# Optimization experiments

Hardware: AMD Instinct MI355X
Metric: run time of the kernel (lower is better)

The kernel has to match this reference:

```python
import jax, jax.numpy as jnp
import numpy as np

N_NODES = 50000


def gcn_conv(x, edge_index, W, b):
    """PyG GCNConv: add self-loops, sym-normalize, out = A_hat @ (x W) + b."""
    src, dst = edge_index[0], edge_index[1]
    n = x.shape[0]
    h = x @ W  # [N, out]
    # degree with self-loops (all edge weights = 1)
    deg = jax.ops.segment_sum(jnp.ones_like(dst, dtype=x.dtype), dst, num_segments=n) + 1.0
    dinv = jax.lax.rsqrt(deg)  # deg >= 1 so safe
    norm = dinv[src] * dinv[dst]  # [E]
    msgs = h[src] * norm[:, None]  # gather + scale
    agg = jax.ops.segment_sum(msgs, dst, num_segments=n)  # scatter-add
    agg = agg + h * (dinv * dinv)[:, None]  # self-loop term: norm_ii = dinv_i^2
    return agg + b


def setup_inputs() -> dict:
    key = jax.random.key(0)
    k_x, k_e, k_w1, k_w2 = jax.random.split(key, 4)
    in_ch, hid, out_ch = 256, 128, 128
    x = jax.random.normal(k_x, (N_NODES, in_ch), dtype=jnp.float32)
    edge_index = jax.random.randint(k_e, (2, 1_600_000), 0, N_NODES, dtype=jnp.int32)
    # Glorot-style init like PyG GCNConv
    W1 = jax.random.normal(k_w1, (in_ch, hid), dtype=jnp.float32) * (1.0 / np.sqrt(in_ch))
    b1 = jnp.zeros((hid,), dtype=jnp.float32)
    W2 = jax.random.normal(k_w2, (hid, out_ch), dtype=jnp.float32) * (1.0 / np.sqrt(hid))
    b2 = jnp.zeros((out_ch,), dtype=jnp.float32)
    return {"x": x, "edge_index": edge_index, "W1": W1, "b1": b1, "W2": W2, "b2": b2}


def reference(x, edge_index, W1, b1, W2, b2):
    # layer 1: GCNConv -> ReLU (dropout is identity in eval mode)
    h = jax.nn.relu(gcn_conv(x, edge_index, W1, b1))
    # layer 2: GCNConv -> ReLU
    out = jax.nn.relu(gcn_conv(h, edge_index, W2, b2))
    return out
```

## Files before the change

### kernel.cpp

```cpp
#include <hip/hip_runtime.h>
#include <cstdint>
#include <cstddef>


#define ELL_STRIDE 64
#define BCAP 8192
#define OVF_CAP 1024
#define PART_T 2048

typedef __attribute__((ext_vector_type(8))) short bf16x8;
typedef __attribute__((ext_vector_type(4))) float floatx4;

__device__ __forceinline__ unsigned short f2bf(float f) {
  unsigned int u = __float_as_uint(f);
  unsigned int r = (u + 0x7fffu + ((u >> 16) & 1u)) >> 16;
  return (unsigned short)r;
}
__device__ __forceinline__ float2 bfpair(unsigned int p) {
  float2 r;
  r.x = __uint_as_float(p << 16);
  r.y = __uint_as_float(p & 0xffff0000u);
  return r;
}

__global__ __launch_bounds__(256) void k_cvt_w(const float* __restrict__ W1,
                                               const float* __restrict__ W2,
                                               unsigned short* __restrict__ WT1,
                                               unsigned short* __restrict__ WT2,
                                               int* __restrict__ cursor,
                                               int* __restrict__ ovf_cnt,
                                               int NB) {
  int i = blockIdx.x * 256 + threadIdx.x;
  if (i < NB) cursor[i] = 0;
  if (i == NB) *ovf_cnt = 0;
  if (i < 128 * 256) {
    int n = i >> 8, k = i & 255;
    WT1[i] = f2bf(W1[k * 128 + n]);
  } else if (i < 128 * 256 + 128 * 128) {
    int j = i - 128 * 256;
    int n = j >> 7, k = j & 127;
    WT2[j] = f2bf(W2[k * 128 + n]);
  }
}

__global__ __launch_bounds__(256) void k_part(const int* __restrict__ src,
                                              const int* __restrict__ dst,
                                              int* __restrict__ cursor,
                                              unsigned int* __restrict__ part,
                                              int* __restrict__ ovf_cnt,
                                              int* __restrict__ ovf,
                                              int E, int NB) {
  __shared__ unsigned int stage1[PART_T];
  __shared__ unsigned int stage2[PART_T];
  __shared__ int hist[512];
  __shared__ int base_g[512];
  __shared__ int base_l[512];
  __shared__ int cl[512];
  __shared__ int sc[256];
  const int tid = threadIdx.x;
  const int e0 = blockIdx.x * PART_T;
  int valid = E - e0; if (valid > PART_T) valid = PART_T;

  hist[tid] = 0; hist[tid + 256] = 0;
  cl[tid] = 0; cl[tid + 256] = 0;
  __syncthreads();
  for (int i = tid; i < valid; i += 256) {
    int e = e0 + i;
    unsigned int v = (unsigned int)(src[e] & 0xffff) | ((unsigned int)dst[e] << 16);
    stage1[i] = v;
    atomicAdd(&hist[(v >> 16) >> 7], 1);
  }
  __syncthreads();
  for (int b = tid; b < NB; b += 256) base_g[b] = atomicAdd(&cursor[b], hist[b]);
  int h0 = hist[2 * tid], h1 = hist[2 * tid + 1];
  int pv = h0 + h1;
  sc[tid] = pv;
  __syncthreads();
  #pragma unroll
  for (int off = 1; off < 256; off <<= 1) {
    int t = (tid >= off) ? sc[tid - off] : 0;
    __syncthreads();
    sc[tid] += t;
    __syncthreads();
  }
  int excl = sc[tid] - pv;
  base_l[2 * tid] = excl;
  base_l[2 * tid + 1] = excl + h0;
  __syncthreads();
  for (int i = tid; i < valid; i += 256) {
    unsigned int v = stage1[i];
    int b = (v >> 16) >> 7;
    int pos = base_l[b] + atomicAdd(&cl[b], 1);
    stage2[pos] = v;
  }
  __syncthreads();
  for (int i = tid; i < valid; i += 256) {
    unsigned int v = stage2[i];
    int b = (v >> 16) >> 7;
    int g = base_g[b] + (i - base_l[b]);
    if (g < BCAP) {
      part[(size_t)b * BCAP + g] = v;
    } else {
      int p = atomicAdd(ovf_cnt, 1);
      if (p < OVF_CAP) { ovf[2 * p] = (int)(v & 0xffffu); ovf[2 * p + 1] = (int)(v >> 16); }
    }
  }
}

__global__ __launch_bounds__(256) void k_fill2(const unsigned int* __restrict__ part,
                                               const int* __restrict__ cursor,
                                               unsigned short* __restrict__ col,
                                               int* __restrict__ cnt,
                                               float* __restrict__ dinv,
                                               int* __restrict__ ovf_cnt,
                                               int* __restrict__ ovf, int N) {
  __shared__ unsigned short slab[128 * ELL_STRIDE];
  __shared__ int cl[128];
  const int tid = threadIdx.x;
  const int b = blockIdx.x;
  if (tid < 128) cl[tid] = 0;
  __syncthreads();
  int count = cursor[b]; if (count > BCAP) count = BCAP;
  const unsigned int* p = part + (size_t)b * BCAP;
  for (int i = tid; i < count; i += 256) {
    unsigned int v = p[i];
    int row = (v >> 16) & 127;
    int k = atomicAdd(&cl[row], 1);
    if (k < ELL_STRIDE) {
      slab[row * ELL_STRIDE + k] = (unsigned short)(v & 0xffffu);
    } else {
      int q = atomicAdd(ovf_cnt, 1);
      if (q < OVF_CAP) { ovf[2 * q] = (int)(v & 0xffffu); ovf[2 * q + 1] = (int)(v >> 16); }
    }
  }
  __syncthreads();
  uint4* d4 = (uint4*)(col + (size_t)b * 128 * ELL_STRIDE);
  const uint4* s4 = (const uint4*)slab;
  #pragma unroll
  for (int i = 0; i < (128 * ELL_STRIDE * 2) / (16 * 256); ++i)
    d4[i * 256 + tid] = s4[i * 256 + tid];
  if (tid < 128) {
    int node = b * 128 + tid;
    if (node < N) {
      int c = cl[tid];
      cnt[node] = c;
      dinv[node] = rsqrtf((float)c + 1.0f);
    }
  }
}

template <int K, bool AF32>
__global__ __launch_bounds__(256) void k_gemm_mfma(const void* __restrict__ Xv,
                                                   const unsigned short* __restrict__ WT,
                                                   const float* __restrict__ dinv,
                                                   unsigned short* __restrict__ hb,
                                                   int M) {
  constexpr int KP = K + 8;
  __shared__ unsigned short Bs[64 * KP];
  const int tid = threadIdx.x;
  const int wave = tid >> 6, lane = tid & 63;
  const int q = lane >> 4, m = lane & 15;
  const int row0 = blockIdx.x * 64 + wave * 16;
  const bool active = row0 < M;
  const int arow = row0 + m;

  floatx4 acc[8];
  #pragma unroll
  for (int nt = 0; nt < 8; ++nt) acc[nt] = (floatx4){0.f, 0.f, 0.f, 0.f};
  bf16x8 af[K / 32];

  #pragma unroll
  for (int half = 0; half < 2; ++half) {
    __syncthreads();
    for (int c = tid; c < 64 * (K / 8); c += 256) {
      int r = c / (K / 8), ko = (c % (K / 8)) * 8;
      *(uint4*)(Bs + r * KP + ko) =
          *(const uint4*)(WT + (size_t)(half * 64 + r) * K + ko);
    }
    __syncthreads();
    if (active) {
      #pragma unroll
      for (int ks = 0; ks < K / 32; ++ks) {
        const int k0 = ks * 32 + q * 8;
        if (half == 0) {
          if (AF32) {
            const float* X = (const float*)Xv;
            float4 a0 = *(const float4*)(X + (size_t)arow * K + k0);
            float4 a1 = *(const float4*)(X + (size_t)arow * K + k0 + 4);
            af[ks] = (bf16x8){(short)f2bf(a0.x), (short)f2bf(a0.y),
                              (short)f2bf(a0.z), (short)f2bf(a0.w),
                              (short)f2bf(a1.x), (short)f2bf(a1.y),
                              (short)f2bf(a1.z), (short)f2bf(a1.w)};
          } else {
            af[ks] = *(const bf16x8*)((const unsigned short*)Xv +
                                      (size_t)arow * K + k0);
          }
        }
        #pragma unroll
        for (int ntl = 0; ntl < 4; ++ntl) {
          bf16x8 bf = *(const bf16x8*)(Bs + (ntl * 16 + m) * KP + k0);
          acc[half * 4 + ntl] =
              __builtin_amdgcn_mfma_f32_16x16x32_bf16(af[ks], bf, acc[half * 4 + ntl],
                                                      0, 0, 0);
        }
      }
    }
  }
  if (!active) return;
  #pragma unroll
  for (int r = 0; r < 4; ++r) {
    int grow = row0 + q * 4 + r;
    float di = dinv[grow];
    #pragma unroll
    for (int nt = 0; nt < 8; ++nt)
      hb[(size_t)grow * 128 + nt * 16 + m] = f2bf(acc[nt][r] * di);
  }
}

template <bool BF16OUT>
__global__ __launch_bounds__(256) void k_agg(const unsigned int* __restrict__ hb,
                                             const int* __restrict__ cnt,
                                             const unsigned short* __restrict__ col,
                                             const float* __restrict__ dinv,
                                             const int* __restrict__ ovf_cnt,
                                             const int* __restrict__ ovf,
                                             const float* __restrict__ bias,
                                             void* __restrict__ outv, int n) {
  const int wave = threadIdx.x >> 6;
  const int lane = threadIdx.x & 63;
  const int d = blockIdx.x * 4 + wave;
  if (d >= n) return;

  float2 acc = bfpair(hb[(size_t)d * 64 + lane]);

  int m = cnt[d]; if (m > ELL_STRIDE) m = ELL_STRIDE;
  const unsigned short* crow = col + (size_t)d * ELL_STRIDE;
  int k = 0;
  for (; k + 16 <= m; k += 16) {
    ushort4 c0 = *(const ushort4*)(crow + k);
    ushort4 c1 = *(const ushort4*)(crow + k + 4);
    ushort4 c2 = *(const ushort4*)(crow + k + 8);
    ushort4 c3 = *(const ushort4*)(crow + k + 12);
    unsigned int p0 = hb[(size_t)c0.x * 64 + lane];
    unsigned int p1 = hb[(size_t)c0.y * 64 + lane];
    unsigned int p2 = hb[(size_t)c0.z * 64 + lane];
    unsigned int p3 = hb[(size_t)c0.w * 64 + lane];
    unsigned int p4 = hb[(size_t)c1.x * 64 + lane];
    unsigned int p5 = hb[(size_t)c1.y * 64 + lane];
    unsigned int p6 = hb[(size_t)c1.z * 64 + lane];
    unsigned int p7 = hb[(size_t)c1.w * 64 + lane];
    unsigned int p8 = hb[(size_t)c2.x * 64 + lane];
    unsigned int p9 = hb[(size_t)c2.y * 64 + lane];
    unsigned int pa = hb[(size_t)c2.z * 64 + lane];
    unsigned int pb = hb[(size_t)c2.w * 64 + lane];
    unsigned int pc = hb[(size_t)c3.x * 64 + lane];
    unsigned int pd = hb[(size_t)c3.y * 64 + lane];
    unsigned int pe = hb[(size_t)c3.z * 64 + lane];
    unsigned int pf = hb[(size_t)c3.w * 64 + lane];
    float2 v0 = bfpair(p0), v1 = bfpair(p1), v2 = bfpair(p2), v3 = bfpair(p3);
    float2 v4 = bfpair(p4), v5 = bfpair(p5), v6 = bfpair(p6), v7 = bfpair(p7);
    acc.x += v0.x + v1.x + v2.x + v3.x + v4.x + v5.x + v6.x + v7.x;
    acc.y += v0.y + v1.y + v2.y + v3.y + v4.y + v5.y + v6.y + v7.y;
    float2 v8 = bfpair(p8), v9 = bfpair(p9), va = bfpair(pa), vb = bfpair(pb);
    float2 vc = bfpair(pc), vd = bfpair(pd), ve = bfpair(pe), vf = bfpair(pf);
    acc.x += v8.x + v9.x + va.x + vb.x + vc.x + vd.x + ve.x + vf.x;
    acc.y += v8.y + v9.y + va.y + vb.y + vc.y + vd.y + ve.y + vf.y;
  }
  for (; k + 8 <= m; k += 8) {
    ushort4 ca = *(const ushort4*)(crow + k);
    ushort4 cb = *(const ushort4*)(crow + k + 4);
    unsigned int p0 = hb[(size_t)ca.x * 64 + lane];
    unsigned int p1 = hb[(size_t)ca.y * 64 + lane];
    unsigned int p2 = hb[(size_t)ca.z * 64 + lane];
    unsigned int p3 = hb[(size_t)ca.w * 64 + lane];
    unsigned int p4 = hb[(size_t)cb.x * 64 + lane];
    unsigned int p5 = hb[(size_t)cb.y * 64 + lane];
    unsigned int p6 = hb[(size_t)cb.z * 64 + lane];
    unsigned int p7 = hb[(size_t)cb.w * 64 + lane];
    float2 v0 = bfpair(p0), v1 = bfpair(p1), v2 = bfpair(p2), v3 = bfpair(p3);
    float2 v4 = bfpair(p4), v5 = bfpair(p5), v6 = bfpair(p6), v7 = bfpair(p7);
    acc.x += v0.x + v1.x + v2.x + v3.x + v4.x + v5.x + v6.x + v7.x;
    acc.y += v0.y + v1.y + v2.y + v3.y + v4.y + v5.y + v6.y + v7.y;
  }
  for (; k < m; ++k) {
    int c = crow[k];
    float2 v = bfpair(hb[(size_t)c * 64 + lane]);
    acc.x += v.x; acc.y += v.y;
  }
  int V = *ovf_cnt; if (V > OVF_CAP) V = OVF_CAP;
  for (int j = 0; j < V; ++j) {
    if (ovf[2 * j + 1] == d) {
      float2 v = bfpair(hb[(size_t)ovf[2 * j] * 64 + lane]);
      acc.x += v.x; acc.y += v.y;
    }
  }
  float di = dinv[d];
  float2 bv = *(const float2*)(bias + lane * 2);
  float rx = di * acc.x + bv.x;
  float ry = di * acc.y + bv.y;
  rx = rx > 0.f ? rx : 0.f;
  ry = ry > 0.f ? ry : 0.f;
  if (BF16OUT) {
    unsigned int pk = (unsigned int)f2bf(rx) | ((unsigned int)f2bf(ry) << 16);
    ((unsigned int*)outv)[(size_t)d * 64 + lane] = pk;
  } else {
    *(float2*)((float*)outv + (size_t)d * 128 + lane * 2) = make_float2(rx, ry);
  }
}

extern "C" void kernel_launch(void* const* d_in, const int* in_sizes, int n_in,
                              void* d_out, int out_size, void* d_ws, size_t ws_size,
                              hipStream_t stream) {
  const float* x  = (const float*)d_in[0];
  const int*   ei = (const int*)d_in[1];
  const float* W1 = (const float*)d_in[2];
  const float* b1 = (const float*)d_in[3];
  const float* W2 = (const float*)d_in[4];
  const float* b2 = (const float*)d_in[5];
  float* out = (float*)d_out;

  const int IN_CH = 256;
  const int N = in_sizes[0] / IN_CH;
  const int E = in_sizes[1] / 2;
  const int NB = (N + 127) >> 7;

  const int* src = ei;
  const int* dst = ei + E;

  char* ws = (char*)d_ws;
  size_t off = 0;
  auto carve = [&](size_t bytes) {
    void* p = ws + off;
    off += (bytes + 255) & ~(size_t)255;
    return p;
  };
  int*            cursor  = (int*)carve((size_t)NB * 4);
  int*            ovf_cnt = (int*)carve(4);
  int*            ovf     = (int*)carve((size_t)OVF_CAP * 2 * 4);
  int*            cnt     = (int*)carve((size_t)N * 4);
  float*          dinv    = (float*)carve((size_t)N * 4);
  unsigned short* col     = (unsigned short*)carve((size_t)N * ELL_STRIDE * 2);
  unsigned short* hb      = (unsigned short*)carve((size_t)N * 128 * 2);
  unsigned short* WT1     = (unsigned short*)carve(128 * 256 * 2);
  unsigned short* WT2     = (unsigned short*)carve(128 * 128 * 2);
  char*           unionp  = (char*)carve((size_t)NB * BCAP * 4);
  unsigned int*   part    = (unsigned int*)unionp;
  unsigned short* aggbuf  = (unsigned short*)unionp;

  k_cvt_w<<<(128 * 256 + 128 * 128 + 255) / 256, 256, 0, stream>>>(
      W1, W2, WT1, WT2, cursor, ovf_cnt, NB);
  k_part <<<(E + PART_T - 1) / PART_T, 256, 0, stream>>>(src, dst, cursor, part,
                                                         ovf_cnt, ovf, E, NB);
  k_fill2<<<NB, 256, 0, stream>>>(part, cursor, col, cnt, dinv, ovf_cnt, ovf, N);

  int gblocks = (N + 63) / 64;
  int ablocks = (N + 3) / 4;
  k_gemm_mfma<256, true ><<<gblocks, 256, 0, stream>>>(x, WT1, dinv, hb, N);
  k_agg<true ><<<ablocks, 256, 0, stream>>>((const unsigned int*)hb, cnt, col, dinv,
                                            ovf_cnt, ovf, b1, aggbuf, N);
  k_gemm_mfma<128, false><<<gblocks, 256, 0, stream>>>(aggbuf, WT2, dinv, hb, N);
  k_agg<false><<<ablocks, 256, 0, stream>>>((const unsigned int*)hb, cnt, col, dinv,
                                            ovf_cnt, ovf, b2, out, N);
}
```

Baseline: 262.5 us.

## Store hidden features in column-chunk slabs and split aggregation per chunk

```diff
diff --git a/kernel.cpp b/kernel.cpp
--- a/kernel.cpp
+++ b/kernel.cpp
@@ -213,7 +213,7 @@
     float di = dinv[grow];
     #pragma unroll
     for (int nt = 0; nt < 8; ++nt)
-      hb[(size_t)grow * 128 + nt * 16 + m] = f2bf(acc[nt][r] * di);
+      hb[(size_t)nt * M * 16 + (size_t)grow * 16 + m] = f2bf(acc[nt][r] * di);
   }
 }
 
@@ -226,85 +226,55 @@
                                              const int* __restrict__ ovf,
                                              const float* __restrict__ bias,
                                              void* __restrict__ outv, int n) {
-  const int wave = threadIdx.x >> 6;
-  const int lane = threadIdx.x & 63;
-  const int d = blockIdx.x * 4 + wave;
+  const int wave = threadIdx.x >> 6, lane = threadIdx.x & 63;
+  const int chunk = blockIdx.x & 7;
+  const int d = (blockIdx.x >> 3) * 4 + wave;
   if (d >= n) return;
-
-  float2 acc = bfpair(hb[(size_t)d * 64 + lane]);
+  const int e = lane >> 3, u = lane & 7;
+  const unsigned int* slab = hb + (size_t)chunk * n * 8;
 
   int m = cnt[d]; if (m > ELL_STRIDE) m = ELL_STRIDE;
-  const unsigned short* crow = col + (size_t)d * ELL_STRIDE;
-  int k = 0;
-  for (; k + 16 <= m; k += 16) {
-    ushort4 c0 = *(const ushort4*)(crow + k);
-    ushort4 c1 = *(const ushort4*)(crow + k + 4);
-    ushort4 c2 = *(const ushort4*)(crow + k + 8);
-    ushort4 c3 = *(const ushort4*)(crow + k + 12);
-    unsigned int p0 = hb[(size_t)c0.x * 64 + lane];
-    unsigned int p1 = hb[(size_t)c0.y * 64 + lane];
-    unsigned int p2 = hb[(size_t)c0.z * 64 + lane];
-    unsigned int p3 = hb[(size_t)c0.w * 64 + lane];
-    unsigned int p4 = hb[(size_t)c1.x * 64 + lane];
-    unsigned int p5 = hb[(size_t)c1.y * 64 + lane];
-    unsigned int p6 = hb[(size_t)c1.z * 64 + lane];
-    unsigned int p7 = hb[(size_t)c1.w * 64 + lane];
-    unsigned int p8 = hb[(size_t)c2.x * 64 + lane];
-    unsigned int p9 = hb[(size_t)c2.y * 64 + lane];
-    unsigned int pa = hb[(size_t)c2.z * 64 + lane];
-    unsigned int pb = hb[(size_t)c2.w * 64 + lane];
-    unsigned int pc = hb[(size_t)c3.x * 64 + lane];
-    unsigned int pd = hb[(size_t)c3.y * 64 + lane];
-    unsigned int pe = hb[(size_t)c3.z * 64 + lane];
-    unsigned int pf = hb[(size_t)c3.w * 64 + lane];
-    float2 v0 = bfpair(p0), v1 = bfpair(p1), v2 = bfpair(p2), v3 = bfpair(p3);
-    float2 v4 = bfpair(p4), v5 = bfpair(p5), v6 = bfpair(p6), v7 = bfpair(p7);
-    acc.x += v0.x + v1.x + v2.x + v3.x + v4.x + v5.x + v6.x + v7.x;
-    acc.y += v0.y + v1.y + v2.y + v3.y + v4.y + v5.y + v6.y + v7.y;
-    float2 v8 = bfpair(p8), v9 = bfpair(p9), va = bfpair(pa), vb = bfpair(pb);
-    float2 vc = bfpair(pc), vd = bfpair(pd), ve = bfpair(pe), vf = bfpair(pf);
-    acc.x += v8.x + v9.x + va.x + vb.x + vc.x + vd.x + ve.x + vf.x;
-    acc.y += v8.y + v9.y + va.y + vb.y + vc.y + vd.y + ve.y + vf.y;
-  }
-  for (; k + 8 <= m; k += 8) {
-    ushort4 ca = *(const ushort4*)(crow + k);
-    ushort4 cb = *(const ushort4*)(crow + k + 4);
-    unsigned int p0 = hb[(size_t)ca.x * 64 + lane];
-    unsigned int p1 = hb[(size_t)ca.y * 64 + lane];
-    unsigned int p2 = hb[(size_t)ca.z * 64 + lane];
-    unsigned int p3 = hb[(size_t)ca.w * 64 + lane];
-    unsigned int p4 = hb[(size_t)cb.x * 64 + lane];
-    unsigned int p5 = hb[(size_t)cb.y * 64 + lane];
-    unsigned int p6 = hb[(size_t)cb.z * 64 + lane];
-    unsigned int p7 = hb[(size_t)cb.w * 64 + lane];
-    float2 v0 = bfpair(p0), v1 = bfpair(p1), v2 = bfpair(p2), v3 = bfpair(p3);
-    float2 v4 = bfpair(p4), v5 = bfpair(p5), v6 = bfpair(p6), v7 = bfpair(p7);
-    acc.x += v0.x + v1.x + v2.x + v3.x + v4.x + v5.x + v6.x + v7.x;
-    acc.y += v0.y + v1.y + v2.y + v3.y + v4.y + v5.y + v6.y + v7.y;
-  }
-  for (; k < m; ++k) {
-    int c = crow[k];
-    float2 v = bfpair(hb[(size_t)c * 64 + lane]);
+  int cv = (lane < m) ? (int)col[(size_t)d * ELL_STRIDE + lane] : d;
+
+  float2 acc = make_float2(0.f, 0.f);
+  if (e == 0) {
+    float2 v = bfpair(slab[(size_t)d * 8 + u]);
     acc.x += v.x; acc.y += v.y;
   }
-  int V = *ovf_cnt; if (V > OVF_CAP) V = OVF_CAP;
-  for (int j = 0; j < V; ++j) {
-    if (ovf[2 * j + 1] == d) {
-      float2 v = bfpair(hb[(size_t)ovf[2 * j] * 64 + lane]);
-      acc.x += v.x; acc.y += v.y;
-    }
-  }
-  float di = dinv[d];
-  float2 bv = *(const float2*)(bias + lane * 2);
-  float rx = di * acc.x + bv.x;
-  float ry = di * acc.y + bv.y;
-  rx = rx > 0.f ? rx : 0.f;
-  ry = ry > 0.f ? ry : 0.f;
-  if (BF16OUT) {
-    unsigned int pk = (unsigned int)f2bf(rx) | ((unsigned int)f2bf(ry) << 16);
-    ((unsigned int*)outv)[(size_t)d * 64 + lane] = pk;
-  } else {
-    *(float2*)((float*)outv + (size_t)d * 128 + lane * 2) = make_float2(rx, ry);
+  for (int k0 = 0; k0 < m; k0 += 16) {
+    int i0 = k0 + e, i1 = k0 + 8 + e;
+    int c0 = __shfl(cv, i0);
+    int c1 = __shfl(cv, i1);
+    unsigned int p0 = slab[(size_t)c0 * 8 + u];
+    unsigned int p1 = slab[(size_t)c1 * 8 + u];
+    float2 v0 = bfpair(p0), v1 = bfpair(p1);
+    if (i0 < m) { acc.x += v0.x; acc.y += v0.y; }
+    if (i1 < m) { acc.x += v1.x; acc.y += v1.y; }
+  }
+  if (e == 0) {
+    int V = *ovf_cnt; if (V > OVF_CAP) V = OVF_CAP;
+    for (int j = 0; j < V; ++j) {
+      if (ovf[2 * j + 1] == d) {
+        float2 v = bfpair(slab[(size_t)ovf[2 * j] * 8 + u]);
+        acc.x += v.x; acc.y += v.y;
+      }
+    }
+  }
+  acc.x += __shfl_xor(acc.x, 8);  acc.y += __shfl_xor(acc.y, 8);
+  acc.x += __shfl_xor(acc.x, 16); acc.y += __shfl_xor(acc.y, 16);
+  acc.x += __shfl_xor(acc.x, 32); acc.y += __shfl_xor(acc.y, 32);
+  if (e == 0) {
+    float di = dinv[d];
+    float2 bv = *(const float2*)(bias + chunk * 16 + 2 * u);
+    float rx = fmaxf(di * acc.x + bv.x, 0.f);
+    float ry = fmaxf(di * acc.y + bv.y, 0.f);
+    if (BF16OUT) {
+      unsigned int pk = (unsigned int)f2bf(rx) | ((unsigned int)f2bf(ry) << 16);
+      ((unsigned int*)outv)[(size_t)d * 64 + chunk * 8 + u] = pk;
+    } else {
+      *(float2*)((float*)outv + (size_t)d * 128 + chunk * 16 + 2 * u) =
+          make_float2(rx, ry);
+    }
   }
 }
 
@@ -354,7 +324,7 @@
   k_fill2<<<NB, 256, 0, stream>>>(part, cursor, col, cnt, dinv, ovf_cnt, ovf, N);
 
   int gblocks = (N + 63) / 64;
-  int ablocks = (N + 3) / 4;
+  int ablocks = 8 * ((N + 3) / 4);
   k_gemm_mfma<256, true ><<<gblocks, 256, 0, stream>>>(x, WT1, dinv, hb, N);
   k_agg<true ><<<ablocks, 256, 0, stream>>>((const unsigned int*)hb, cnt, col, dinv,
                                             ovf_cnt, ovf, b1, aggbuf, N);
```

New measurement: 389.4 us. 48.3% more time.
